# Optimization experiments

Hardware: AMD Instinct MI355X
Metric: run time of the kernel (lower is better)

Reference implementation:

```python
import jax, jax.numpy as jnp
import numpy as np

DMODEL = 2048
NUM_HEADS = 16
NUM_KV_HEADS = 4
HEAD_DIM = DMODEL // NUM_HEADS  # 128
THETA = 10000.0


def setup_inputs() -> dict:
    key = jax.random.key(0)
    k0, k1, k2, k3, k4 = jax.random.split(key, 5)
    B, S = 1, 4096
    x = jax.random.normal(k0, (B, S, DMODEL), dtype=jnp.float32)
    # Linear weights stored as [in, out] (equivalent to torch [out,in] with x @ W.T)
    sd = 0.02
    wq = jax.random.normal(k1, (DMODEL, NUM_HEADS * HEAD_DIM), dtype=jnp.float32) * sd
    wk = jax.random.normal(k2, (DMODEL, NUM_KV_HEADS * HEAD_DIM), dtype=jnp.float32) * sd
    wv = jax.random.normal(k3, (DMODEL, NUM_KV_HEADS * HEAD_DIM), dtype=jnp.float32) * sd
    wo = jax.random.normal(k4, (NUM_HEADS * HEAD_DIM, DMODEL), dtype=jnp.float32) * sd
    return {"x": x, "wq": wq, "wk": wk, "wv": wv, "wo": wo}


def _rope_cos_sin(seqlen, dtype):
    # RoPE.forward: inv_freq over half the head dim, emb = cat(freqs, freqs)
    inv_freq = 1.0 / (THETA ** (jnp.arange(0, HEAD_DIM, 2, dtype=jnp.float32) / HEAD_DIM))
    pos = jnp.arange(seqlen, dtype=jnp.float32)
    freqs = pos[:, None] * inv_freq[None, :]          # [S, HEAD_DIM/2]
    emb = jnp.concatenate([freqs, freqs], axis=-1)    # [S, HEAD_DIM]
    return emb.astype(dtype) * 0 + jnp.cos(emb).astype(dtype), jnp.sin(emb).astype(dtype)


def _rot(t):
    half = t.shape[-1] // 2
    return jnp.concatenate([-t[..., half:], t[..., :half]], axis=-1)


def reference(x, wq, wk, wv, wo):
    B, S, _ = x.shape
    q = (x @ wq).reshape(B, S, NUM_HEADS, HEAD_DIM).transpose(0, 2, 1, 3)      # [B,H,S,D]
    k = (x @ wk).reshape(B, S, NUM_KV_HEADS, HEAD_DIM).transpose(0, 2, 1, 3)   # [B,KV,S,D]
    v = (x @ wv).reshape(B, S, NUM_KV_HEADS, HEAD_DIM).transpose(0, 2, 1, 3)

    cos, sin = _rope_cos_sin(S, x.dtype)  # [S, D]
    cos = cos[None, None, :, :]
    sin = sin[None, None, :, :]
    q = q * cos + _rot(q) * sin
    k = k * cos + _rot(k) * sin

    rep = NUM_HEADS // NUM_KV_HEADS
    k = jnp.repeat(k, rep, axis=1)  # [B,H,S,D]
    v = jnp.repeat(v, rep, axis=1)

    scale = 1.0 / jnp.sqrt(jnp.asarray(HEAD_DIM, dtype=x.dtype))
    scores = jnp.einsum('bhqd,bhkd->bhqk', q, k) * scale
    causal = jnp.tril(jnp.ones((S, S), dtype=bool))
    scores = jnp.where(causal[None, None], scores, jnp.finfo(x.dtype).min)
    attn = jax.nn.softmax(scores, axis=-1)
    o = jnp.einsum('bhqk,bhkd->bhqd', attn, v)          # [B,H,S,D]
    o = o.transpose(0, 2, 1, 3).reshape(B, S, NUM_HEADS * HEAD_DIM)
    return o @ wo
```

## Files before the change

kernel.cpp:

```cpp
#include <hip/hip_runtime.h>
#include <math.h>

#define SEQ   4096
#define DM    2048
#define NH    16
#define NKV   4
#define HD    128
#define QKVN  3072
#define CEXP  0.12753643f

typedef _Float16 f16;
typedef _Float16 f16x8 __attribute__((ext_vector_type(8)));
typedef _Float16 f16x4v __attribute__((ext_vector_type(4)));
typedef float    f32x4 __attribute__((ext_vector_type(4)));

#define GLD16(g, l) __builtin_amdgcn_global_load_lds(                        \
    (const __attribute__((address_space(1))) unsigned int*)(g),              \
    (__attribute__((address_space(3))) unsigned int*)(l), 16, 0, 0)

__global__ __launch_bounds__(256) void cast_f32_f16_k(const float* __restrict__ in,
                                                      f16* __restrict__ out, int n4)
{
    int i = blockIdx.x * 256 + threadIdx.x;
    if (i >= n4) return;
    float4 v = ((const float4*)in)[i];
    f16x4v h = {(f16)v.x, (f16)v.y, (f16)v.z, (f16)v.w};
    ((f16x4v*)out)[i] = h;
}

__global__ __launch_bounds__(256) void transpose_cast_k(const float* __restrict__ in,
                                                        f16* __restrict__ out,
                                                        int R, int Cn, float scale)
{
    __shared__ float tile[32][33];
    int bx = blockIdx.x * 32, by = blockIdx.y * 32;
    int tx = threadIdx.x & 31, ty = threadIdx.x >> 5;
    #pragma unroll
    for (int i = 0; i < 32; i += 8)
        tile[ty + i][tx] = in[(size_t)(by + ty + i) * Cn + bx + tx];
    __syncthreads();
    #pragma unroll
    for (int i = 0; i < 32; i += 8)
        out[(size_t)(bx + ty + i) * R + by + tx] = (f16)(tile[tx][ty + i] * scale);
}

__global__ __launch_bounds__(256) void transpose_f16_k(const f16* __restrict__ in,
                                                       f16* __restrict__ out,
                                                       int R, int Cn, int ldin)
{
    __shared__ f16 tile[32][33];
    int bx = blockIdx.x * 32, by = blockIdx.y * 32;
    int tx = threadIdx.x & 31, ty = threadIdx.x >> 5;
    #pragma unroll
    for (int i = 0; i < 32; i += 8)
        tile[ty + i][tx] = in[(size_t)(by + ty + i) * ldin + bx + tx];
    __syncthreads();
    #pragma unroll
    for (int i = 0; i < 32; i += 8)
        out[(size_t)(bx + ty + i) * R + by + tx] = tile[tx][ty + i];
}

template <typename OutT>
__global__ __launch_bounds__(256) void gemm_bt(const f16* __restrict__ A,
                                               const f16* __restrict__ Bt,
                                               OutT* __restrict__ C,
                                               int M, int N, int K)
{
    __shared__ __align__(16) f16 sm[16384];
    f16* As = sm;
    f16* Bs = sm + 8192;

    const int t = threadIdx.x;
    const int w = t >> 6;
    const int lane = t & 63, ln = lane & 15, quad = lane >> 4;
    const size_t bm = (size_t)blockIdx.y * 128, bn = (size_t)blockIdx.x * 128;
    const int wm = (w >> 1) * 64, wn = (w & 1) * 64;

    int srow[4], scol[4];
    #pragma unroll
    for (int cc = 0; cc < 4; ++cc) {
        int pos = cc * 256 + t;
        srow[cc] = pos >> 3;
        scol[cc] = ((pos & 7) ^ (srow[cc] & 7)) * 8;
    }

    f32x4 acc[4][4];
    #pragma unroll
    for (int i = 0; i < 4; ++i)
        #pragma unroll
        for (int j = 0; j < 4; ++j) acc[i][j] = (f32x4){0.f, 0.f, 0.f, 0.f};

    for (int k0 = 0; k0 < K; k0 += 64) {
        #pragma unroll
        for (int cc = 0; cc < 4; ++cc) {
            GLD16(A  + (bm + srow[cc]) * (size_t)K + k0 + scol[cc],
                  As + (cc * 256 + w * 64) * 8);
            GLD16(Bt + (bn + srow[cc]) * (size_t)K + k0 + scol[cc],
                  Bs + (cc * 256 + w * 64) * 8);
        }
        __syncthreads();

        #pragma unroll
        for (int tt = 0; tt < 2; ++tt) {
            const int ch = ((tt * 4 + quad) ^ (ln & 7)) * 8;
            f16x8 af[4], bf[4];
            #pragma unroll
            for (int i = 0; i < 4; ++i) {
                af[i] = *(const f16x8*)&As[(wm + i * 16 + ln) * 64 + ch];
                bf[i] = *(const f16x8*)&Bs[(wn + i * 16 + ln) * 64 + ch];
            }
            #pragma unroll
            for (int i = 0; i < 4; ++i)
                #pragma unroll
                for (int j = 0; j < 4; ++j)
                    acc[i][j] = __builtin_amdgcn_mfma_f32_16x16x32_f16(af[i], bf[j], acc[i][j], 0, 0, 0);
        }
        __syncthreads();
    }

    #pragma unroll
    for (int i = 0; i < 4; ++i)
        #pragma unroll
        for (int j = 0; j < 4; ++j)
            #pragma unroll
            for (int r = 0; r < 4; ++r)
                C[(bm + wm + i * 16 + quad * 4 + r) * (size_t)N + bn + wn + j * 16 + ln]
                    = (OutT)acc[i][j][r];
}

__global__ __launch_bounds__(256) void rope_k(f16* __restrict__ qkv)
{
    const int s = blockIdx.x, t = threadIdx.x;
    for (int p = t; p < (NH + NKV) * 64; p += 256) {
        int hh = p >> 6, i = p & 63;
        f16* base = (hh < NH) ? qkv + (size_t)s * QKVN + hh * HD
                              : qkv + (size_t)s * QKVN + DM + (hh - NH) * HD;
        float inv = __builtin_exp2f((float)i * -0.20762050f);
        float ang = (float)s * inv;
        float c = cosf(ang), sn = sinf(ang);
        float x0 = (float)base[i], x1 = (float)base[i + 64];
        base[i]      = (f16)(x0 * c - x1 * sn);
        base[i + 64] = (f16)(x1 * c + x0 * sn);
    }
}

__global__ __launch_bounds__(256, 2) void flash_k(const f16* __restrict__ qkv,
                                                  const f16* __restrict__ vt,
                                                  f16* __restrict__ O0,
                                                  f16* __restrict__ O1,
                                                  float* __restrict__ lpart)
{
    const int bid  = blockIdx.x;
    const int xcd  = bid & 7;
    const int rr   = bid >> 3;
    const int kvh  = xcd >> 1;
    const int h    = kvh * 4 + (xcd & 1) * 2 + (rr & 1);
    const int px   = (rr >> 1) & 15;
    const int half = rr >> 5;

    const int t = threadIdx.x, w = t >> 6, lane = t & 63, ln = lane & 15, quad = lane >> 4;

    f16*   Op = half ? O1 : O0;
    float* lp = lpart + (size_t)half * NH * SEQ + (size_t)h * SEQ;

    __shared__ __align__(16) f16 sm[40960];
    f16* Ps = sm + 32768 + w * 2048;

    const int glo = half * 33;
    const int ghi = glo + 33;

    int krow[4], kc[4], vrow[4], vc[4];
    #pragma unroll
    for (int cc = 0; cc < 4; ++cc) {
        int pos = cc * 256 + t;
        krow[cc] = pos >> 4; kc[cc] = (pos & 15) ^ (krow[cc] & 15);
        vrow[cc] = pos >> 3; vc[cc] = (pos & 7) ^ (vrow[cc] & 7);
    }

    #pragma unroll
    for (int ph = 0; ph < 2; ++ph) {
        const int bx   = ph ? (31 - px) : px;
        const int q0   = bx * 128;
        const int ntp  = 2 * bx + 2;
        const int base = ph ? (2 * px + 2) : 0;
        int tb_lo = glo - base; if (tb_lo < 0) tb_lo = 0;
        int tb_hi = ghi - base; if (tb_hi > ntp) tb_hi = ntp;

        const f16* kp[4]; const f16* vp[4];
        #pragma unroll
        for (int cc = 0; cc < 4; ++cc) {
            kp[cc] = qkv + (size_t)(tb_lo * 64 + krow[cc]) * QKVN + DM + kvh * HD + kc[cc] * 8;
            vp[cc] = vt  + (size_t)(kvh * HD + vrow[cc]) * SEQ + tb_lo * 64 + vc[cc] * 8;
        }
        auto stage = [&](int b) {
            f16* Kd = sm + b * 8192;
            f16* Vd = sm + 16384 + b * 8192;
            #pragma unroll
            for (int cc = 0; cc < 4; ++cc) {
                GLD16(kp[cc], Kd + (cc * 256 + t) * 8);
                GLD16(vp[cc], Vd + (cc * 256 + t) * 8);
                kp[cc] += 64 * QKVN;
                vp[cc] += 64;
            }
        };

        f16x8 qf[2][4];
        #pragma unroll
        for (int rf = 0; rf < 2; ++rf) {
            const f16* qrow = qkv + (size_t)(q0 + w * 32 + rf * 16 + ln) * QKVN + h * HD;
            #pragma unroll
            for (int tt = 0; tt < 4; ++tt)
                qf[rf][tt] = *(const f16x8*)(qrow + tt * 32 + quad * 8);
        }

        float l_r[2][4] = {{0.f, 0.f, 0.f, 0.f}, {0.f, 0.f, 0.f, 0.f}};
        f32x4 oacc[2][8];
        #pragma unroll
        for (int rf = 0; rf < 2; ++rf)
            #pragma unroll
            for (int dt = 0; dt < 8; ++dt) oacc[rf][dt] = (f32x4){0.f, 0.f, 0.f, 0.f};

        if (tb_lo < tb_hi) stage(0);
        __syncthreads();

        for (int tb = tb_lo; tb < tb_hi; ++tb) {
            const int cur = (tb - tb_lo) & 1;
            if (tb + 1 < tb_hi) stage(cur ^ 1);

            const f16* Ks  = sm + cur * 8192;
            const f16* Vts = sm + 16384 + cur * 8192;

            f32x4 sacc[2][4];
            #pragma unroll
            for (int rf = 0; rf < 2; ++rf)
                #pragma unroll
                for (int c2 = 0; c2 < 4; ++c2) sacc[rf][c2] = (f32x4){0.f, 0.f, 0.f, 0.f};
            #pragma unroll
            for (int tt = 0; tt < 4; ++tt) {
                #pragma unroll
                for (int c2 = 0; c2 < 4; ++c2) {
                    f16x8 bk = *(const f16x8*)&Ks[(c2 * 16 + ln) * 128 + ((tt * 4 + quad) ^ ln) * 8];
                    sacc[0][c2] = __builtin_amdgcn_mfma_f32_16x16x32_f16(qf[0][tt], bk, sacc[0][c2], 0, 0, 0);
                    sacc[1][c2] = __builtin_amdgcn_mfma_f32_16x16x32_f16(qf[1][tt], bk, sacc[1][c2], 0, 0, 0);
                }
            }

            if (tb >= ntp - 2) {
                const int ko = (tb - (ntp - 2)) * 64;
                #pragma unroll
                for (int rf = 0; rf < 2; ++rf)
                    #pragma unroll
                    for (int c2 = 0; c2 < 4; ++c2)
                        #pragma unroll
                        for (int r = 0; r < 4; ++r)
                            if (ko + c2 * 16 + ln > w * 32 + rf * 16 + quad * 4 + r)
                                sacc[rf][c2][r] = -INFINITY;
            }

            #pragma unroll
            for (int rf = 0; rf < 2; ++rf)
                #pragma unroll
                for (int c2 = 0; c2 < 4; ++c2)
                    #pragma unroll
                    for (int r = 0; r < 4; ++r) {
                        float e = __builtin_exp2f(sacc[rf][c2][r]);
                        l_r[rf][r] += e;
                        int row = rf * 16 + quad * 4 + r;
                        int slot = (c2 * 2 + (ln >> 3)) ^ (row & 7);
                        Ps[row * 64 + slot * 8 + (ln & 7)] = (f16)e;
                    }

            #pragma unroll
            for (int t2 = 0; t2 < 2; ++t2) {
                f16x8 pa0 = *(const f16x8*)&Ps[(0 * 16 + ln) * 64 + ((t2 * 4 + quad) ^ (ln & 7)) * 8];
                f16x8 pa1 = *(const f16x8*)&Ps[(1 * 16 + ln) * 64 + ((t2 * 4 + quad) ^ (ln & 7)) * 8];
                #pragma unroll
                for (int dt = 0; dt < 8; ++dt) {
                    f16x8 bv = *(const f16x8*)&Vts[(dt * 16 + ln) * 64 + ((t2 * 4 + quad) ^ (ln & 7)) * 8];
                    oacc[0][dt] = __builtin_amdgcn_mfma_f32_16x16x32_f16(pa0, bv, oacc[0][dt], 0, 0, 0);
                    oacc[1][dt] = __builtin_amdgcn_mfma_f32_16x16x32_f16(pa1, bv, oacc[1][dt], 0, 0, 0);
                }
            }

            __syncthreads();
        }

        #pragma unroll
        for (int rf = 0; rf < 2; ++rf)
            #pragma unroll
            for (int r = 0; r < 4; ++r) {
                float l = l_r[rf][r];
                l += __shfl_xor(l, 1, 64);
                l += __shfl_xor(l, 2, 64);
                l += __shfl_xor(l, 4, 64);
                l += __shfl_xor(l, 8, 64);
                if (ln == 0)
                    lp[q0 + w * 32 + rf * 16 + quad * 4 + r] = l;
            }
        #pragma unroll
        for (int rf = 0; rf < 2; ++rf)
            #pragma unroll
            for (int dt = 0; dt < 8; ++dt)
                #pragma unroll
                for (int r = 0; r < 4; ++r)
                    Op[(size_t)(q0 + w * 32 + rf * 16 + quad * 4 + r) * DM + h * HD + dt * 16 + ln]
                        = (f16)oacc[rf][dt][r];
    }
}

__global__ __launch_bounds__(256) void merge_k(const f16* __restrict__ O0,
                                               const f16* __restrict__ O1,
                                               const float* __restrict__ l0,
                                               const float* __restrict__ l1,
                                               f16* __restrict__ oh)
{
    int idx = blockIdx.x * 256 + threadIdx.x;
    int row = idx >> 8;
    int hh  = (idx & 255) >> 4;
    float li = 1.0f / (l0[hh * SEQ + row] + l1[hh * SEQ + row]);
    f16x8 a = ((const f16x8*)O0)[idx];
    f16x8 b = ((const f16x8*)O1)[idx];
    f16x8 o;
    #pragma unroll
    for (int i = 0; i < 8; ++i)
        o[i] = (f16)(((float)a[i] + (float)b[i]) * li);
    ((f16x8*)oh)[idx] = o;
}

extern "C" void kernel_launch(void* const* d_in, const int* in_sizes, int n_in,
                              void* d_out, int out_size, void* d_ws, size_t ws_size,
                              hipStream_t stream)
{
    (void)in_sizes; (void)n_in; (void)out_size; (void)ws_size;
    const float* x  = (const float*)d_in[0];
    const float* wq = (const float*)d_in[1];
    const float* wk = (const float*)d_in[2];
    const float* wv = (const float*)d_in[3];
    const float* wo = (const float*)d_in[4];
    float* out = (float*)d_out;

    f16* xh    = (f16*)d_ws;
    f16* wtqkv = xh + 8388608ull;
    f16* wot   = wtqkv + 6291456ull;
    f16* qkvb  = wot + 4194304ull;
    f16* vtb   = qkvb + 12582912ull;
    f16* O1    = vtb + 2097152ull;
    f16* O0    = xh;
    f16* oh    = xh;
    float* lbuf = (float*)wtqkv;

    cast_f32_f16_k<<<8192, 256, 0, stream>>>(x, xh, 2097152);
    transpose_cast_k<<<dim3(64, 64), 256, 0, stream>>>(wq, wtqkv, 2048, 2048, CEXP);
    transpose_cast_k<<<dim3(16, 64), 256, 0, stream>>>(wk, wtqkv + 2048ull * 2048, 2048, 512, 1.0f);
    transpose_cast_k<<<dim3(16, 64), 256, 0, stream>>>(wv, wtqkv + 2560ull * 2048, 2048, 512, 1.0f);
    transpose_cast_k<<<dim3(64, 64), 256, 0, stream>>>(wo, wot, 2048, 2048, 1.0f);

    gemm_bt<f16><<<dim3(24, 32), 256, 0, stream>>>(xh, wtqkv, qkvb, 4096, 3072, 2048);
    rope_k<<<4096, 256, 0, stream>>>(qkvb);
    transpose_f16_k<<<dim3(16, 128), 256, 0, stream>>>(qkvb + 2560, vtb, 4096, 512, 3072);
    flash_k<<<dim3(512), 256, 0, stream>>>(qkvb, vtb, O0, O1, lbuf);
    merge_k<<<4096, 256, 0, stream>>>(O0, O1, lbuf, lbuf + (size_t)NH * SEQ, oh);
    gemm_bt<float><<<dim3(16, 32), 256, 0, stream>>>(oh, wot, out, 4096, 2048, 2048);
}
```

Measured before the change: 345.4 us.

## Replace GEMM with 8-wave double-buffered 256-row tile pipeline

Replaces the simple 128x128 single-buffer GEMM with a 512-thread kernel that computes 256xBN tiles. Global-to-LDS loads for the next k-tile are split into quarters and interleaved with MFMA phases over double-buffered LDS, using partial vmcnt waits, scheduling barriers and setprio. The aim is to hide load latency and raise data reuse in both the QKV and output projections. In exchange it needs much more LDS per block and launches far fewer blocks, 192 for the QKV GEMM, so some CUs may sit idle.

```diff
diff --git a/kernel.cpp b/kernel.cpp
--- a/kernel.cpp
+++ b/kernel.cpp
@@ -60,71 +60,119 @@
         out[(size_t)(bx + ty + i) * R + by + tx] = tile[tx][ty + i];
 }
 
-template <typename OutT>
-__global__ __launch_bounds__(256) void gemm_bt(const f16* __restrict__ A,
-                                               const f16* __restrict__ Bt,
-                                               OutT* __restrict__ C,
-                                               int M, int N, int K)
-{
-    __shared__ __align__(16) f16 sm[16384];
+template <int BN, typename OutT>
+__global__ __launch_bounds__(512, 2) void gemm8p(const f16* __restrict__ A,
+                                                 const f16* __restrict__ Bt,
+                                                 OutT* __restrict__ C,
+                                                 int M, int N, int K)
+{
+    constexpr int LB  = (BN == 256) ? 2 : 1;
+    constexpr int NF  = BN / 16;
+    constexpr int NPP = NF / 4;
+    (void)M;
+
+    __shared__ __align__(16) f16 sm[32768 + 2 * BN * 64];
     f16* As = sm;
-    f16* Bs = sm + 8192;
+    f16* Bs = sm + 32768;
 
     const int t = threadIdx.x;
     const int w = t >> 6;
     const int lane = t & 63, ln = lane & 15, quad = lane >> 4;
-    const size_t bm = (size_t)blockIdx.y * 128, bn = (size_t)blockIdx.x * 128;
-    const int wm = (w >> 1) * 64, wn = (w & 1) * 64;
-
-    int srow[4], scol[4];
-    #pragma unroll
-    for (int cc = 0; cc < 4; ++cc) {
-        int pos = cc * 256 + t;
-        srow[cc] = pos >> 3;
-        scol[cc] = ((pos & 7) ^ (srow[cc] & 7)) * 8;
+    const size_t bm = (size_t)blockIdx.y * 256, bn = (size_t)blockIdx.x * BN;
+
+    auto stageA = [&](int half, int nb, size_t kn) {
+        #pragma unroll
+        for (int cc = 0; cc < 2; ++cc) {
+            int pos = cc * 512 + t;
+            int rl  = pos >> 3;
+            int sc  = (pos & 7) ^ (rl & 7);
+            GLD16(A + (bm + half * 128 + rl) * (size_t)K + kn + sc * 8,
+                  As + nb * 16384 + half * 8192 + pos * 8);
+        }
+    };
+    auto stageB = [&](int half, int nb, size_t kn) {
+        #pragma unroll
+        for (int cc = 0; cc < LB; ++cc) {
+            int pos = cc * 512 + t;
+            int rl  = pos >> 3;
+            int sc  = (pos & 7) ^ (rl & 7);
+            GLD16(Bt + (bn + half * (BN / 2) + rl) * (size_t)K + kn + sc * 8,
+                  Bs + nb * (BN * 64) + half * (BN * 32) + pos * 8);
+        }
+    };
+
+    f32x4 acc[2][NF];
+    #pragma unroll
+    for (int i = 0; i < 2; ++i)
+        #pragma unroll
+        for (int j = 0; j < NF; ++j) acc[i][j] = (f32x4){0.f, 0.f, 0.f, 0.f};
+
+    const int KT = K >> 6;
+
+    stageA(0, 0, 0); stageA(1, 0, 0); stageB(0, 0, 0); stageB(1, 0, 0);
+    asm volatile("s_waitcnt vmcnt(0)" ::: "memory");
+    __builtin_amdgcn_s_barrier();
+
+    f16x8 af[2][2];
+
+    for (int kt = 0; kt < KT; ++kt) {
+        const int b = kt & 1, nb = b ^ 1;
+        const size_t kn = (size_t)((kt + 1 < KT) ? (kt + 1) * 64 : (KT - 1) * 64);
+        const int Ab = b * 16384, Bb = b * (BN * 64);
+
+        #pragma unroll
+        for (int q = 0; q < 4; ++q) {
+            if (q == 0) {
+                #pragma unroll
+                for (int i = 0; i < 2; ++i)
+                    #pragma unroll
+                    for (int kk = 0; kk < 2; ++kk)
+                        af[i][kk] = *(const f16x8*)&As[Ab + (w * 32 + i * 16 + ln) * 64
+                                                         + ((kk * 4 + quad) ^ (ln & 7)) * 8];
+            }
+            f16x8 bf[NPP][2];
+            #pragma unroll
+            for (int jj = 0; jj < NPP; ++jj)
+                #pragma unroll
+                for (int kk = 0; kk < 2; ++kk)
+                    bf[jj][kk] = *(const f16x8*)&Bs[Bb + ((q * NPP + jj) * 16 + ln) * 64
+                                                       + ((kk * 4 + quad) ^ (ln & 7)) * 8];
+
+            if (q == 0) stageA(0, nb, kn);
+            if (q == 1) stageA(1, nb, kn);
+            if (q == 2) stageB(0, nb, kn);
+            if (q == 3) stageB(1, nb, kn);
+
+            if (q == 1) asm volatile("s_waitcnt vmcnt(4)" ::: "memory");
+            if (q == 3) {
+                if constexpr (LB == 2) asm volatile("s_waitcnt vmcnt(2)" ::: "memory");
+                else                   asm volatile("s_waitcnt vmcnt(1)" ::: "memory");
+            }
+
+            __builtin_amdgcn_sched_barrier(0);
+            __builtin_amdgcn_s_barrier();
+            __builtin_amdgcn_sched_barrier(0);
+            __builtin_amdgcn_s_setprio(1);
+            #pragma unroll
+            for (int jj = 0; jj < NPP; ++jj)
+                #pragma unroll
+                for (int i = 0; i < 2; ++i)
+                    #pragma unroll
+                    for (int kk = 0; kk < 2; ++kk)
+                        acc[i][q * NPP + jj] = __builtin_amdgcn_mfma_f32_16x16x32_f16(
+                            af[i][kk], bf[jj][kk], acc[i][q * NPP + jj], 0, 0, 0);
+            __builtin_amdgcn_s_setprio(0);
+            __builtin_amdgcn_sched_barrier(0);
+        }
     }
 
-    f32x4 acc[4][4];
-    #pragma unroll
-    for (int i = 0; i < 4; ++i)
-        #pragma unroll
-        for (int j = 0; j < 4; ++j) acc[i][j] = (f32x4){0.f, 0.f, 0.f, 0.f};
-
-    for (int k0 = 0; k0 < K; k0 += 64) {
-        #pragma unroll
-        for (int cc = 0; cc < 4; ++cc) {
-            GLD16(A  + (bm + srow[cc]) * (size_t)K + k0 + scol[cc],
-                  As + (cc * 256 + w * 64) * 8);
-            GLD16(Bt + (bn + srow[cc]) * (size_t)K + k0 + scol[cc],
-                  Bs + (cc * 256 + w * 64) * 8);
-        }
-        __syncthreads();
-
-        #pragma unroll
-        for (int tt = 0; tt < 2; ++tt) {
-            const int ch = ((tt * 4 + quad) ^ (ln & 7)) * 8;
-            f16x8 af[4], bf[4];
-            #pragma unroll
-            for (int i = 0; i < 4; ++i) {
-                af[i] = *(const f16x8*)&As[(wm + i * 16 + ln) * 64 + ch];
-                bf[i] = *(const f16x8*)&Bs[(wn + i * 16 + ln) * 64 + ch];
-            }
-            #pragma unroll
-            for (int i = 0; i < 4; ++i)
-                #pragma unroll
-                for (int j = 0; j < 4; ++j)
-                    acc[i][j] = __builtin_amdgcn_mfma_f32_16x16x32_f16(af[i], bf[j], acc[i][j], 0, 0, 0);
-        }
-        __syncthreads();
-    }
-
-    #pragma unroll
-    for (int i = 0; i < 4; ++i)
-        #pragma unroll
-        for (int j = 0; j < 4; ++j)
+    #pragma unroll
+    for (int i = 0; i < 2; ++i)
+        #pragma unroll
+        for (int j = 0; j < NF; ++j)
             #pragma unroll
             for (int r = 0; r < 4; ++r)
-                C[(bm + wm + i * 16 + quad * 4 + r) * (size_t)N + bn + wn + j * 16 + ln]
+                C[(bm + w * 32 + i * 16 + quad * 4 + r) * (size_t)N + bn + j * 16 + ln]
                     = (OutT)acc[i][j][r];
 }
 
@@ -355,10 +403,10 @@
     transpose_cast_k<<<dim3(16, 64), 256, 0, stream>>>(wv, wtqkv + 2560ull * 2048, 2048, 512, 1.0f);
     transpose_cast_k<<<dim3(64, 64), 256, 0, stream>>>(wo, wot, 2048, 2048, 1.0f);
 
-    gemm_bt<f16><<<dim3(24, 32), 256, 0, stream>>>(xh, wtqkv, qkvb, 4096, 3072, 2048);
+    gemm8p<256, f16><<<dim3(12, 16), 512, 0, stream>>>(xh, wtqkv, qkvb, 4096, 3072, 2048);
     rope_k<<<4096, 256, 0, stream>>>(qkvb);
     transpose_f16_k<<<dim3(16, 128), 256, 0, stream>>>(qkvb + 2560, vtb, 4096, 512, 3072);
     flash_k<<<dim3(512), 256, 0, stream>>>(qkvb, vtb, O0, O1, lbuf);
     merge_k<<<4096, 256, 0, stream>>>(O0, O1, lbuf, lbuf + (size_t)NH * SEQ, oh);
-    gemm_bt<float><<<dim3(16, 32), 256, 0, stream>>>(oh, wot, out, 4096, 2048, 2048);
-}
+    gemm8p<128, float><<<dim3(16, 16), 512, 0, stream>>>(oh, wot, out, 4096, 2048, 2048);
+}
```

After: 327.6 us. 1.05x faster.
